# Kernel tuning notes

Measured on AMD Instinct MI355X. Metric: run time of the kernel, lower is better.

The kernel has to match this reference:

```python
import jax, jax.numpy as jnp
import numpy as np

N_NODES = 50000
N_EDGES = 800000
IN_DIM = 1200   # latent_size * num_heads
OUT_DIM = 300
NEG_SLOPE = 0.2  # PyG GATConv default


def setup_inputs() -> dict:
    key = jax.random.key(0)
    k1, k2, k3, k4, k5 = jax.random.split(key, 5)
    z = jax.random.normal(k1, (N_NODES, IN_DIM), dtype=jnp.float32)
    edge_index = jax.random.randint(k2, (2, N_EDGES), 0, N_NODES, dtype=jnp.int64)
    # GATConv params (heads=1): lin weight [out, in], attention vectors [out], bias [out]
    W = jax.random.normal(k3, (OUT_DIM, IN_DIM), dtype=jnp.float32) * (1.0 / np.sqrt(IN_DIM))
    att_src = jax.random.normal(k4, (OUT_DIM,), dtype=jnp.float32) * 0.1
    att_dst = jax.random.normal(k5, (OUT_DIM,), dtype=jnp.float32) * 0.1
    bias = jnp.zeros((OUT_DIM,), dtype=jnp.float32)
    return {"z": z, "edge_index": edge_index, "W": W,
            "att_src": att_src, "att_dst": att_dst, "bias": bias}


def reference(z, edge_index, W, att_src, att_dst, bias):
    N = z.shape[0]
    # Linear projection (no bias on lin in GATConv; bias added after aggregation)
    x = z @ W.T                                   # [N, OUT_DIM]
    # add self-loops (GATConv default add_self_loops=True)
    loop = jnp.arange(N, dtype=edge_index.dtype)
    src = jnp.concatenate([edge_index[0], loop])  # message source j
    dst = jnp.concatenate([edge_index[1], loop])  # message target i
    # per-node attention logits
    a_src = x @ att_src                           # [N]
    a_dst = x @ att_dst                           # [N]
    # per-edge score, softmax over incoming edges of each target node
    e = jax.nn.leaky_relu(a_src[src] + a_dst[dst], negative_slope=NEG_SLOPE)  # [E+N]
    e_max = jax.ops.segment_max(e, dst, num_segments=N)   # every node has a self-loop
    ex = jnp.exp(e - e_max[dst])
    denom = jax.ops.segment_sum(ex, dst, num_segments=N)
    alpha = ex / denom[dst]                       # [E+N]
    # weighted aggregation (scatter-add over targets)
    out = jax.ops.segment_sum(alpha[:, None] * x[src], dst, num_segments=N)
    return out + bias
```

## Files before the change

### kernel.cpp

```cpp
#include <hip/hip_runtime.h>

#define N_NODES 50000
#define N_EDGES 800000
#define IN_DIM  1200
#define KP      1216
#define OUT_DIM 300
#define BNP     320
#define XBS     304
#define BM      64
#define NKT     38
#define GRID_M  ((N_NODES + BM - 1) / BM)

typedef __attribute__((ext_vector_type(8))) short short8;
typedef __attribute__((ext_vector_type(4))) float f32x4;

__device__ __forceinline__ short f2bf(float f) {
  unsigned u = __builtin_bit_cast(unsigned, f);
  u += 0x7fffu + ((u >> 16) & 1u);
  return (short)(u >> 16);
}
__device__ __forceinline__ float bf2f(unsigned short h) {
  return __builtin_bit_cast(float, (unsigned)h << 16);
}
__device__ __forceinline__ float lrelu(float v) { return v > 0.f ? v : 0.2f * v; }

__device__ __forceinline__ float wredMaxF(float v) {
  #pragma unroll
  for (int o = 32; o > 0; o >>= 1) v = fmaxf(v, __shfl_xor(v, o));
  return v;
}
__device__ __forceinline__ float wredSumF(float v) {
  #pragma unroll
  for (int o = 32; o > 0; o >>= 1) v += __shfl_xor(v, o);
  return v;
}

__device__ __forceinline__ void gl_lds16(const unsigned short* g, unsigned short* l) {
  __builtin_amdgcn_global_load_lds(
      (const __attribute__((address_space(1))) unsigned int*)g,
      (__attribute__((address_space(3))) unsigned int*)l, 16, 0, 0);
}

__global__ __launch_bounds__(256) void wconv(const float* __restrict__ W,
                                             unsigned short* __restrict__ Wb) {
  int f = blockIdx.x * 256 + threadIdx.x;
  if (f >= BNP * KP / 8) return;
  int n = (f * 8) / KP, c = (f * 8) % KP;
  short8 v = {0,0,0,0,0,0,0,0};
  if (n < OUT_DIM && c < IN_DIM) {
    const float4* p = reinterpret_cast<const float4*>(W + (size_t)n * IN_DIM + c);
    float4 f0 = p[0], f1 = p[1];
    v[0]=f2bf(f0.x); v[1]=f2bf(f0.y); v[2]=f2bf(f0.z); v[3]=f2bf(f0.w);
    v[4]=f2bf(f1.x); v[5]=f2bf(f1.y); v[6]=f2bf(f1.z); v[7]=f2bf(f1.w);
  }
  *reinterpret_cast<short8*>(&Wb[(size_t)n * KP + c]) = v;
}

__global__ __launch_bounds__(256) void gemm_x(const float* __restrict__ z,
                                              const unsigned short* __restrict__ Wb,
                                              const float* __restrict__ att_s,
                                              const float* __restrict__ att_d,
                                              unsigned short* __restrict__ xb,
                                              float* __restrict__ a_s,
                                              float* __restrict__ a_d) {
  __shared__ __align__(16) unsigned short As[2][BM * 32];
  __shared__ __align__(16) unsigned short Bs[2][BNP * 32];

  const int tid  = threadIdx.x;
  const int lane = tid & 63;
  const int wid  = tid >> 6;
  const int lr   = lane & 15;
  const int lg   = lane >> 4;
  const int lrs  = (lr >> 1) & 3;
  const int m0   = blockIdx.x * BM;

  f32x4 zero4 = {0.f, 0.f, 0.f, 0.f};
  const float4 fz4 = make_float4(0.f, 0.f, 0.f, 0.f);
  f32x4 acc[4][5];
  #pragma unroll
  for (int mf = 0; mf < 4; ++mf)
    #pragma unroll
    for (int nj = 0; nj < 5; ++nj) acc[mf][nj] = zero4;

  const int ra  = tid >> 2;
  const int kaL = tid & 3;
  const int kaP = kaL ^ ((ra >> 1) & 3);
  const int am  = m0 + ra;
  float4 ga0, ga1;

  const int brow = wid * 16 + (lane >> 2);
  const int bgc  = (lane & 3) ^ ((lane >> 3) & 3);

  #define LOADA(KT)                                                           \
    {                                                                         \
      int k = (KT) * 32 + kaL * 8;                                            \
      if (am < N_NODES && k + 8 <= IN_DIM) {                                  \
        const float4* p = reinterpret_cast<const float4*>(z + (size_t)am * IN_DIM + k); \
        ga0 = p[0]; ga1 = p[1];                                               \
      } else { ga0 = fz4; ga1 = fz4; }                                        \
    }

  #define WRITEA(BUF)                                                         \
    {                                                                         \
      short8 v;                                                               \
      v[0]=f2bf(ga0.x); v[1]=f2bf(ga0.y); v[2]=f2bf(ga0.z); v[3]=f2bf(ga0.w); \
      v[4]=f2bf(ga1.x); v[5]=f2bf(ga1.y); v[6]=f2bf(ga1.z); v[7]=f2bf(ga1.w); \
      *reinterpret_cast<short8*>(&As[BUF][ra * 32 + kaP * 8]) = v;            \
    }

  #define STAGEB(BUF, KT)                                                     \
    _Pragma("unroll")                                                         \
    for (int j = 0; j < 5; ++j) {                                             \
      const unsigned short* gsrc =                                            \
          Wb + (size_t)(j * 64 + brow) * KP + (KT) * 32 + bgc * 8;            \
      unsigned short* ldst = &Bs[BUF][(j * 64 + wid * 16) * 32];              \
      gl_lds16(gsrc, ldst);                                                   \
    }

  STAGEB(0, 0);
  LOADA(0);
  WRITEA(0);
  __syncthreads();

  #pragma unroll 1
  for (int kt = 0; kt < NKT; ++kt) {
    const int cur = kt & 1;
    if (kt < NKT - 1) {
      STAGEB(cur ^ 1, kt + 1);
      LOADA(kt + 1);
    }

    short8 a[4];
    #pragma unroll
    for (int mf = 0; mf < 4; ++mf)
      a[mf] = *reinterpret_cast<const short8*>(
          &As[cur][(mf * 16 + lr) * 32 + (lg ^ lrs) * 8]);
    #pragma unroll
    for (int nj = 0; nj < 5; ++nj) {
      short8 b = *reinterpret_cast<const short8*>(
          &Bs[cur][(wid * 80 + nj * 16 + lr) * 32 + (lg ^ lrs) * 8]);
      #pragma unroll
      for (int mf = 0; mf < 4; ++mf)
        acc[mf][nj] = __builtin_amdgcn_mfma_f32_16x16x32_bf16(a[mf], b, acc[mf][nj], 0, 0, 0);
    }

    if (kt < NKT - 1) { WRITEA(cur ^ 1); }
    __syncthreads();
  }
  #undef LOADA
  #undef WRITEA
  #undef STAGEB

  float* red = reinterpret_cast<float*>(&As[0][0]);

  float ps[4][4], pd[4][4];
  #pragma unroll
  for (int mf = 0; mf < 4; ++mf)
    #pragma unroll
    for (int jj = 0; jj < 4; ++jj) { ps[mf][jj] = 0.f; pd[mf][jj] = 0.f; }

  #pragma unroll
  for (int nj = 0; nj < 5; ++nj) {
    int c = wid * 80 + nj * 16 + lr;
    bool cv = c < OUT_DIM;
    float vs = cv ? att_s[c] : 0.f;
    float vd = cv ? att_d[c] : 0.f;
    #pragma unroll
    for (int mf = 0; mf < 4; ++mf) {
      #pragma unroll
      for (int jj = 0; jj < 4; ++jj) {
        float val = acc[mf][nj][jj];
        int r = m0 + mf * 16 + 4 * lg + jj;
        if (cv && r < N_NODES) xb[(size_t)r * XBS + c] = (unsigned short)f2bf(val);
        ps[mf][jj] += val * vs;
        pd[mf][jj] += val * vd;
      }
    }
  }
  #pragma unroll
  for (int mf = 0; mf < 4; ++mf)
    #pragma unroll
    for (int jj = 0; jj < 4; ++jj) {
      #pragma unroll
      for (int o = 8; o > 0; o >>= 1) {
        ps[mf][jj] += __shfl_xor(ps[mf][jj], o);
        pd[mf][jj] += __shfl_xor(pd[mf][jj], o);
      }
      if (lr == 0) {
        int rr = mf * 16 + 4 * lg + jj;
        red[wid * 64 + rr]       = ps[mf][jj];
        red[256 + wid * 64 + rr] = pd[mf][jj];
      }
    }
  __syncthreads();
  if (tid < 64) {
    int r = m0 + tid;
    if (r < N_NODES)
      a_s[r] = red[tid] + red[64 + tid] + red[128 + tid] + red[192 + tid];
  } else if (tid < 128) {
    int t = tid - 64, r = m0 + t;
    if (r < N_NODES)
      a_d[r] = red[256 + t] + red[256 + 64 + t] + red[256 + 128 + t] + red[256 + 192 + t];
  }
}

__global__ void hist(const int* __restrict__ ei, int* __restrict__ deg) {
  int e = blockIdx.x * blockDim.x + threadIdx.x;
  if (e < N_EDGES) {
    unsigned dst = (unsigned)ei[N_EDGES + e];
    if (dst < N_NODES) atomicAdd(&deg[dst], 1);
  }
}

#define SCAN_B 1024
#define NBLK   49

__global__ __launch_bounds__(SCAN_B) void scan1(const int* __restrict__ deg,
                                                int* __restrict__ bsum) {
  int i = blockIdx.x * SCAN_B + threadIdx.x;
  int v = (i < N_NODES) ? deg[i] : 0;
  #pragma unroll
  for (int o = 32; o > 0; o >>= 1) v += __shfl_xor(v, o);
  __shared__ int wt[16];
  if ((threadIdx.x & 63) == 0) wt[threadIdx.x >> 6] = v;
  __syncthreads();
  if (threadIdx.x == 0) {
    int t = 0;
    #pragma unroll
    for (int w = 0; w < 16; ++w) t += wt[w];
    bsum[blockIdx.x] = t;
  }
}

__global__ void scan2(const int* __restrict__ bsum, int* __restrict__ bex,
                      int* __restrict__ offs) {
  int l = threadIdx.x;
  int v = (l < NBLK) ? bsum[l] : 0;
  int incl = v;
  #pragma unroll
  for (int off = 1; off < 64; off <<= 1) {
    int u = __shfl_up(incl, off);
    if (l >= off) incl += u;
  }
  if (l < NBLK) bex[l] = incl - v;
  if (l == NBLK - 1) offs[N_NODES] = incl;
}

__global__ __launch_bounds__(SCAN_B) void scan3(const int* __restrict__ deg,
                                                const int* __restrict__ bex,
                                                int* __restrict__ offs,
                                                int* __restrict__ cursor) {
  int tid = threadIdx.x;
  int i = blockIdx.x * SCAN_B + tid;
  int lane = tid & 63, wid = tid >> 6;
  int v = (i < N_NODES) ? deg[i] : 0;
  int incl = v;
  #pragma unroll
  for (int off = 1; off < 64; off <<= 1) {
    int u = __shfl_up(incl, off);
    if (lane >= off) incl += u;
  }
  __shared__ int wt[16];
  if (lane == 63) wt[wid] = incl;
  __syncthreads();
  if (tid < 16) {
    int t = wt[tid];
    int sc = t;
    #pragma unroll
    for (int off = 1; off < 16; off <<= 1) {
      int u = __shfl_up(sc, off);
      if (tid >= off) sc += u;
    }
    wt[tid] = sc - t;
  }
  __syncthreads();
  int excl = incl - v + wt[wid] + bex[blockIdx.x];
  if (i < N_NODES) { offs[i] = excl; cursor[i] = excl; }
}

__global__ void fill(const int* __restrict__ ei, int* __restrict__ cursor,
                     int* __restrict__ srcs) {
  int e = blockIdx.x * blockDim.x + threadIdx.x;
  if (e < N_EDGES) {
    unsigned dst = (unsigned)ei[N_EDGES + e];
    unsigned src = (unsigned)ei[e];
    if (dst < N_NODES && src < N_NODES) {
      int pos = atomicAdd(&cursor[dst], 1);
      srcs[pos] = (int)src;
    }
  }
}

__global__ __launch_bounds__(256) void minv_k(const float* __restrict__ a_s,
                                              const float* __restrict__ a_d,
                                              const int* __restrict__ offs,
                                              const int* __restrict__ srcs,
                                              float2* __restrict__ minv) {
  int node = blockIdx.x * 4 + (threadIdx.x >> 6);
  if (node >= N_NODES) return;
  int lane = threadIdx.x & 63;
  int beg = offs[node], end = offs[node + 1];
  float adi = a_d[node];
  float eself = lrelu(a_s[node] + adi);

  float m = eself;
  for (int k = beg + lane; k < end; k += 64)
    m = fmaxf(m, lrelu(a_s[srcs[k]] + adi));
  m = wredMaxF(m);

  float s = 0.f;
  for (int k = beg + lane; k < end; k += 64)
    s += expf(lrelu(a_s[srcs[k]] + adi) - m);
  s = wredSumF(s) + expf(eself - m);
  if (lane == 0) minv[node] = make_float2(m, 1.0f / s);
}

#define CCH 15
__global__ __launch_bounds__(256) void aggregate(const unsigned short* __restrict__ xb,
                                                 const float* __restrict__ a_s,
                                                 const float* __restrict__ a_d,
                                                 const float2* __restrict__ minv,
                                                 const int* __restrict__ offs,
                                                 const int* __restrict__ srcs,
                                                 const float* __restrict__ bias,
                                                 float* __restrict__ out) {
  unsigned wi = blockIdx.x * 256u + threadIdx.x;
  if (wi >= (unsigned)N_NODES * CCH) return;
  unsigned node = wi / CCH;
  unsigned cc = wi - node * CCH;

  int beg = offs[node], end = offs[node + 1];
  float2 mi = minv[node];
  const float m = mi.x, inv = mi.y;
  const float adi = a_d[node];
  const float wself = expf(lrelu(a_s[node] + adi) - m) * inv;

  const unsigned short* xcol = xb + 20u * cc;

  float acc[20];
  {
    const unsigned short* xr = xcol + (size_t)node * XBS;
    #pragma unroll
    for (int q = 0; q < 5; ++q) {
      ushort4 xv = *reinterpret_cast<const ushort4*>(xr + 4 * q);
      acc[4*q+0] = wself * bf2f(xv.x);
      acc[4*q+1] = wself * bf2f(xv.y);
      acc[4*q+2] = wself * bf2f(xv.z);
      acc[4*q+3] = wself * bf2f(xv.w);
    }
  }

  for (int k = beg; k < end; ++k) {
    int sj = srcs[k];
    float w = expf(lrelu(a_s[sj] + adi) - m) * inv;
    const unsigned short* xr = xcol + (size_t)sj * XBS;
    #pragma unroll
    for (int q = 0; q < 5; ++q) {
      ushort4 xv = *reinterpret_cast<const ushort4*>(xr + 4 * q);
      acc[4*q+0] += w * bf2f(xv.x);
      acc[4*q+1] += w * bf2f(xv.y);
      acc[4*q+2] += w * bf2f(xv.z);
      acc[4*q+3] += w * bf2f(xv.w);
    }
  }
  float* op = out + (size_t)node * OUT_DIM + 20u * cc;
  const float* bp = bias + 20u * cc;
  #pragma unroll
  for (int q = 0; q < 5; ++q) {
    float4 b = *reinterpret_cast<const float4*>(bp + 4 * q);
    float4 o = {acc[4*q] + b.x, acc[4*q+1] + b.y, acc[4*q+2] + b.z, acc[4*q+3] + b.w};
    *reinterpret_cast<float4*>(op + 4 * q) = o;
  }
}

extern "C" void kernel_launch(void* const* d_in, const int* in_sizes, int n_in,
                              void* d_out, int out_size, void* d_ws, size_t ws_size,
                              hipStream_t stream) {
  const float* z     = (const float*)d_in[0];
  const int*   ei    = (const int*)d_in[1];
  const float* W     = (const float*)d_in[2];
  const float* att_s = (const float*)d_in[3];
  const float* att_d = (const float*)d_in[4];
  const float* bias  = (const float*)d_in[5];
  float* out = (float*)d_out;

  char* ws = (char*)d_ws;
  size_t off = 0;
  unsigned short* xb = (unsigned short*)(ws + off); off += (size_t)N_NODES * XBS * 2;
  unsigned short* Wb = (unsigned short*)(ws + off); off += (size_t)BNP * KP * 2;
  float*  a_s  = (float*)(ws + off);  off += 50048 * 4;
  float*  a_d  = (float*)(ws + off);  off += 50048 * 4;
  int*    deg  = (int*)(ws + off);    off += 50048 * 4;
  int*    offs = (int*)(ws + off);    off += 50056 * 4;
  int*    cur  = (int*)(ws + off);    off += 50048 * 4;
  int*    bsum = (int*)(ws + off);    off += 64 * 4;
  int*    bex  = (int*)(ws + off);    off += 64 * 4;
  int*    srcs = (int*)(ws + off);    off += (size_t)N_EDGES * 4;
  float2* minv = (float2*)(ws + off); off += (size_t)50048 * 8;

  (void)hipMemsetAsync(deg, 0, N_NODES * 4, stream);

  wconv<<<(BNP * KP / 8 + 255) / 256, 256, 0, stream>>>(W, Wb);
  gemm_x<<<GRID_M, 256, 0, stream>>>(z, Wb, att_s, att_d, xb, a_s, a_d);
  hist<<<(N_EDGES + 255) / 256, 256, 0, stream>>>(ei, deg);
  scan1<<<NBLK, SCAN_B, 0, stream>>>(deg, bsum);
  scan2<<<1, 64, 0, stream>>>(bsum, bex, offs);
  scan3<<<NBLK, SCAN_B, 0, stream>>>(deg, bex, offs, cur);
  fill<<<(N_EDGES + 255) / 256, 256, 0, stream>>>(ei, cur, srcs);
  minv_k<<<(N_NODES + 3) / 4, 256, 0, stream>>>(a_s, a_d, offs, srcs, minv);
  aggregate<<<((unsigned)N_NODES * CCH + 255) / 256, 256, 0, stream>>>(
      xb, a_s, a_d, minv, offs, srcs, bias, out);
}
```

Before: 329.3 us.

## Deepen GEMM pipeline with two-tile A register prefetch and manual waitcnt barriers

Restructures the projection GEMM main loop into a manually unrolled two-stage ping-pong where global A loads run two k-tiles ahead in alternating register sets. __syncthreads is replaced by explicit s_waitcnt vmcnt(2) plus s_barrier, so the latest A prefetch can stay in flight across the barrier. Out-of-range loads become clamped unconditional loads with zero-masking applied at the LDS write. The aim is to hide global-load latency behind MFMA work. In exchange it uses more registers and depends on hand-counted vmcnt values being correct.

```diff
diff --git a/kernel.cpp b/kernel.cpp
--- a/kernel.cpp
+++ b/kernel.cpp
@@ -86,25 +86,28 @@
   const int kaL = tid & 3;
   const int kaP = kaL ^ ((ra >> 1) & 3);
   const int am  = m0 + ra;
-  float4 ga0, ga1;
-
-  const int brow = wid * 16 + (lane >> 2);
-  const int bgc  = (lane & 3) ^ ((lane >> 3) & 3);
-
-  #define LOADA(KT)                                                           \
+  const int amc = am < N_NODES ? am : N_NODES - 1;
+  const bool mok = am < N_NODES;
+
+  float4 gA0, gA1, gB0, gB1;
+
+  const int bgc = (lane & 3) ^ ((lane >> 3) & 3);
+
+  #define LOADA(G0, G1, KT)                                                   \
     {                                                                         \
       int k = (KT) * 32 + kaL * 8;                                            \
-      if (am < N_NODES && k + 8 <= IN_DIM) {                                  \
-        const float4* p = reinterpret_cast<const float4*>(z + (size_t)am * IN_DIM + k); \
-        ga0 = p[0]; ga1 = p[1];                                               \
-      } else { ga0 = fz4; ga1 = fz4; }                                        \
-    }
-
-  #define WRITEA(BUF)                                                         \
+      int kc = k > (IN_DIM - 8) ? (IN_DIM - 8) : k;                           \
+      const float4* p = reinterpret_cast<const float4*>(z + (size_t)amc * IN_DIM + kc); \
+      G0 = p[0]; G1 = p[1];                                                   \
+    }
+
+  #define WRITEA(BUF, G0, G1, KT)                                             \
     {                                                                         \
+      bool ok = mok && ((KT) * 32 + kaL * 8 + 8 <= IN_DIM);                   \
+      float4 f0 = ok ? G0 : fz4, f1 = ok ? G1 : fz4;                          \
       short8 v;                                                               \
-      v[0]=f2bf(ga0.x); v[1]=f2bf(ga0.y); v[2]=f2bf(ga0.z); v[3]=f2bf(ga0.w); \
-      v[4]=f2bf(ga1.x); v[5]=f2bf(ga1.y); v[6]=f2bf(ga1.z); v[7]=f2bf(ga1.w); \
+      v[0]=f2bf(f0.x); v[1]=f2bf(f0.y); v[2]=f2bf(f0.z); v[3]=f2bf(f0.w);     \
+      v[4]=f2bf(f1.x); v[5]=f2bf(f1.y); v[6]=f2bf(f1.z); v[7]=f2bf(f1.w);     \
       *reinterpret_cast<short8*>(&As[BUF][ra * 32 + kaP * 8]) = v;            \
     }
 
@@ -112,44 +115,75 @@
     _Pragma("unroll")                                                         \
     for (int j = 0; j < 5; ++j) {                                             \
       const unsigned short* gsrc =                                            \
-          Wb + (size_t)(j * 64 + brow) * KP + (KT) * 32 + bgc * 8;            \
-      unsigned short* ldst = &Bs[BUF][(j * 64 + wid * 16) * 32];              \
-      gl_lds16(gsrc, ldst);                                                   \
-    }
-
+          Wb + (size_t)(j * 64 + wid * 16 + (lane >> 2)) * KP + (KT) * 32 + bgc * 8; \
+      gl_lds16(gsrc, &Bs[BUF][(j * 64 + wid * 16) * 32]);                     \
+    }
+
+  #define COMPUTE(CUR)                                                        \
+    {                                                                         \
+      short8 a0_ = *reinterpret_cast<const short8*>(&As[CUR][(lr) * 32 + (lg ^ lrs) * 8]);        \
+      short8 a1_ = *reinterpret_cast<const short8*>(&As[CUR][(16 + lr) * 32 + (lg ^ lrs) * 8]);   \
+      short8 a2_ = *reinterpret_cast<const short8*>(&As[CUR][(32 + lr) * 32 + (lg ^ lrs) * 8]);   \
+      short8 a3_ = *reinterpret_cast<const short8*>(&As[CUR][(48 + lr) * 32 + (lg ^ lrs) * 8]);   \
+      _Pragma("unroll")                                                       \
+      for (int nj = 0; nj < 5; ++nj) {                                        \
+        short8 b = *reinterpret_cast<const short8*>(                          \
+            &Bs[CUR][(wid * 80 + nj * 16 + lr) * 32 + (lg ^ lrs) * 8]);       \
+        acc[0][nj] = __builtin_amdgcn_mfma_f32_16x16x32_bf16(a0_, b, acc[0][nj], 0, 0, 0); \
+        acc[1][nj] = __builtin_amdgcn_mfma_f32_16x16x32_bf16(a1_, b, acc[1][nj], 0, 0, 0); \
+        acc[2][nj] = __builtin_amdgcn_mfma_f32_16x16x32_bf16(a2_, b, acc[2][nj], 0, 0, 0); \
+        acc[3][nj] = __builtin_amdgcn_mfma_f32_16x16x32_bf16(a3_, b, acc[3][nj], 0, 0, 0); \
+      }                                                                       \
+    }
+
+  #define FENCE asm volatile("" ::: "memory")
+  #define CBAR  asm volatile("s_waitcnt vmcnt(2) lgkmcnt(0)" ::: "memory");   \
+                __builtin_amdgcn_s_barrier();                                 \
+                asm volatile("" ::: "memory")
+
+  LOADA(gA0, gA1, 0);
+  FENCE;
   STAGEB(0, 0);
-  LOADA(0);
-  WRITEA(0);
-  __syncthreads();
+  FENCE;
+  LOADA(gB0, gB1, 1);
+  FENCE;
+  WRITEA(0, gA0, gA1, 0);
+  CBAR;
 
   #pragma unroll 1
-  for (int kt = 0; kt < NKT; ++kt) {
-    const int cur = kt & 1;
-    if (kt < NKT - 1) {
-      STAGEB(cur ^ 1, kt + 1);
-      LOADA(kt + 1);
-    }
-
-    short8 a[4];
-    #pragma unroll
-    for (int mf = 0; mf < 4; ++mf)
-      a[mf] = *reinterpret_cast<const short8*>(
-          &As[cur][(mf * 16 + lr) * 32 + (lg ^ lrs) * 8]);
-    #pragma unroll
-    for (int nj = 0; nj < 5; ++nj) {
-      short8 b = *reinterpret_cast<const short8*>(
-          &Bs[cur][(wid * 80 + nj * 16 + lr) * 32 + (lg ^ lrs) * 8]);
-      #pragma unroll
-      for (int mf = 0; mf < 4; ++mf)
-        acc[mf][nj] = __builtin_amdgcn_mfma_f32_16x16x32_bf16(a[mf], b, acc[mf][nj], 0, 0, 0);
-    }
-
-    if (kt < NKT - 1) { WRITEA(cur ^ 1); }
-    __syncthreads();
-  }
+  for (int kt = 0; kt < 36; kt += 2) {
+    STAGEB(1, kt + 1);
+    FENCE;
+    LOADA(gA0, gA1, kt + 2);
+    FENCE;
+    COMPUTE(0);
+    WRITEA(1, gB0, gB1, kt + 1);
+    CBAR;
+
+    STAGEB(0, kt + 2);
+    FENCE;
+    LOADA(gB0, gB1, kt + 3);
+    FENCE;
+    COMPUTE(1);
+    WRITEA(0, gA0, gA1, kt + 2);
+    CBAR;
+  }
+
+  STAGEB(1, 37);
+  FENCE;
+  COMPUTE(0);
+  WRITEA(1, gB0, gB1, 37);
+  __syncthreads();
+
+  COMPUTE(1);
+  __syncthreads();
+
   #undef LOADA
   #undef WRITEA
   #undef STAGEB
+  #undef COMPUTE
+  #undef FENCE
+  #undef CBAR
 
   float* red = reinterpret_cast<float*>(&As[0][0]);
 
```

Result: slower. 338.6 us (+2.8%).

## Double GEMM row tile to 128 with 8 waves sharing each staged W tile

Applied to the files above, without the earlier changes.

The projection GEMM now uses 128-row blocks with 512 threads arranged as 2 row-waves by 4 column-waves. Each staged B (weight) tile in LDS is reused across twice as many rows, which halves the number of blocks and the total W traffic from global memory. B staging is redistributed across the 8 waves, and the attention-logit reduction is re-indexed for 128 rows. This costs a larger A buffer in LDS and fewer blocks (391), which may leave the GPU's compute units unevenly loaded.

```diff
diff --git a/kernel.cpp b/kernel.cpp
--- a/kernel.cpp
+++ b/kernel.cpp
@@ -7,7 +7,7 @@
 #define OUT_DIM 300
 #define BNP     320
 #define XBS     304
-#define BM      64
+#define BM      128
 #define NKT     38
 #define GRID_M  ((N_NODES + BM - 1) / BM)
 
@@ -56,7 +56,7 @@
   *reinterpret_cast<short8*>(&Wb[(size_t)n * KP + c]) = v;
 }
 
-__global__ __launch_bounds__(256) void gemm_x(const float* __restrict__ z,
+__global__ __launch_bounds__(512) void gemm_x(const float* __restrict__ z,
                                               const unsigned short* __restrict__ Wb,
                                               const float* __restrict__ att_s,
                                               const float* __restrict__ att_d,
@@ -69,6 +69,8 @@
   const int tid  = threadIdx.x;
   const int lane = tid & 63;
   const int wid  = tid >> 6;
+  const int mw   = wid >> 2;
+  const int nw   = wid & 3;
   const int lr   = lane & 15;
   const int lg   = lane >> 4;
   const int lrs  = (lr >> 1) & 3;
@@ -88,8 +90,7 @@
   const int am  = m0 + ra;
   float4 ga0, ga1;
 
-  const int brow = wid * 16 + (lane >> 2);
-  const int bgc  = (lane & 3) ^ ((lane >> 3) & 3);
+  const int bgc = (lane & 3) ^ ((lane >> 3) & 3);
 
   #define LOADA(KT)                                                           \
     {                                                                         \
@@ -110,11 +111,13 @@
 
   #define STAGEB(BUF, KT)                                                     \
     _Pragma("unroll")                                                         \
-    for (int j = 0; j < 5; ++j) {                                             \
-      const unsigned short* gsrc =                                            \
-          Wb + (size_t)(j * 64 + brow) * KP + (KT) * 32 + bgc * 8;            \
-      unsigned short* ldst = &Bs[BUF][(j * 64 + wid * 16) * 32];              \
-      gl_lds16(gsrc, ldst);                                                   \
+    for (int t5 = 0; t5 < 3; ++t5) {                                          \
+      int j = wid + 8 * t5;                                                   \
+      if (j < 20) {                                                           \
+        const unsigned short* gsrc =                                          \
+            Wb + (size_t)(j * 16 + (lane >> 2)) * KP + (KT) * 32 + bgc * 8;   \
+        gl_lds16(gsrc, &Bs[BUF][j * 16 * 32]);                                \
+      }                                                                       \
     }
 
   STAGEB(0, 0);
@@ -130,18 +133,18 @@
       LOADA(kt + 1);
     }
 
-    short8 a[4];
-    #pragma unroll
-    for (int mf = 0; mf < 4; ++mf)
-      a[mf] = *reinterpret_cast<const short8*>(
-          &As[cur][(mf * 16 + lr) * 32 + (lg ^ lrs) * 8]);
+    short8 a0 = *reinterpret_cast<const short8*>(&As[cur][(mw * 64 +      lr) * 32 + (lg ^ lrs) * 8]);
+    short8 a1 = *reinterpret_cast<const short8*>(&As[cur][(mw * 64 + 16 + lr) * 32 + (lg ^ lrs) * 8]);
+    short8 a2 = *reinterpret_cast<const short8*>(&As[cur][(mw * 64 + 32 + lr) * 32 + (lg ^ lrs) * 8]);
+    short8 a3 = *reinterpret_cast<const short8*>(&As[cur][(mw * 64 + 48 + lr) * 32 + (lg ^ lrs) * 8]);
     #pragma unroll
     for (int nj = 0; nj < 5; ++nj) {
       short8 b = *reinterpret_cast<const short8*>(
-          &Bs[cur][(wid * 80 + nj * 16 + lr) * 32 + (lg ^ lrs) * 8]);
-      #pragma unroll
-      for (int mf = 0; mf < 4; ++mf)
-        acc[mf][nj] = __builtin_amdgcn_mfma_f32_16x16x32_bf16(a[mf], b, acc[mf][nj], 0, 0, 0);
+          &Bs[cur][(nw * 80 + nj * 16 + lr) * 32 + (lg ^ lrs) * 8]);
+      acc[0][nj] = __builtin_amdgcn_mfma_f32_16x16x32_bf16(a0, b, acc[0][nj], 0, 0, 0);
+      acc[1][nj] = __builtin_amdgcn_mfma_f32_16x16x32_bf16(a1, b, acc[1][nj], 0, 0, 0);
+      acc[2][nj] = __builtin_amdgcn_mfma_f32_16x16x32_bf16(a2, b, acc[2][nj], 0, 0, 0);
+      acc[3][nj] = __builtin_amdgcn_mfma_f32_16x16x32_bf16(a3, b, acc[3][nj], 0, 0, 0);
     }
 
     if (kt < NKT - 1) { WRITEA(cur ^ 1); }
@@ -161,7 +164,7 @@
 
   #pragma unroll
   for (int nj = 0; nj < 5; ++nj) {
-    int c = wid * 80 + nj * 16 + lr;
+    int c = nw * 80 + nj * 16 + lr;
     bool cv = c < OUT_DIM;
     float vs = cv ? att_s[c] : 0.f;
     float vd = cv ? att_d[c] : 0.f;
@@ -170,7 +173,7 @@
       #pragma unroll
       for (int jj = 0; jj < 4; ++jj) {
         float val = acc[mf][nj][jj];
-        int r = m0 + mf * 16 + 4 * lg + jj;
+        int r = m0 + mw * 64 + mf * 16 + 4 * lg + jj;
         if (cv && r < N_NODES) xb[(size_t)r * XBS + c] = (unsigned short)f2bf(val);
         ps[mf][jj] += val * vs;
         pd[mf][jj] += val * vd;
@@ -187,20 +190,20 @@
         pd[mf][jj] += __shfl_xor(pd[mf][jj], o);
       }
       if (lr == 0) {
-        int rr = mf * 16 + 4 * lg + jj;
-        red[wid * 64 + rr]       = ps[mf][jj];
-        red[256 + wid * 64 + rr] = pd[mf][jj];
+        int rr = mw * 64 + mf * 16 + 4 * lg + jj;
+        red[nw * 128 + rr]       = ps[mf][jj];
+        red[512 + nw * 128 + rr] = pd[mf][jj];
       }
     }
   __syncthreads();
-  if (tid < 64) {
+  if (tid < 128) {
     int r = m0 + tid;
     if (r < N_NODES)
-      a_s[r] = red[tid] + red[64 + tid] + red[128 + tid] + red[192 + tid];
-  } else if (tid < 128) {
-    int t = tid - 64, r = m0 + t;
+      a_s[r] = red[tid] + red[128 + tid] + red[256 + tid] + red[384 + tid];
+  } else if (tid < 256) {
+    int t = tid - 128, r = m0 + t;
     if (r < N_NODES)
-      a_d[r] = red[256 + t] + red[256 + 64 + t] + red[256 + 128 + t] + red[256 + 192 + t];
+      a_d[r] = red[512 + t] + red[512 + 128 + t] + red[512 + 256 + t] + red[512 + 384 + t];
   }
 }
 
@@ -401,7 +404,7 @@
   (void)hipMemsetAsync(deg, 0, N_NODES * 4, stream);
 
   wconv<<<(BNP * KP / 8 + 255) / 256, 256, 0, stream>>>(W, Wb);
-  gemm_x<<<GRID_M, 256, 0, stream>>>(z, Wb, att_s, att_d, xb, a_s, a_d);
+  gemm_x<<<GRID_M, 512, 0, stream>>>(z, Wb, att_s, att_d, xb, a_s, a_d);
   hist<<<(N_EDGES + 255) / 256, 256, 0, stream>>>(ei, deg);
   scan1<<<NBLK, SCAN_B, 0, stream>>>(deg, bsum);
   scan2<<<1, 64, 0, stream>>>(bsum, bex, offs);
```

Result: no change. 332.0 us (+0.8%).

## Load W fragments directly from global and shrink GEMM M-tile to 48

Applied to the files above, without the earlier changes.

The projection GEMM no longer stages the bf16 weight tile in LDS with global_load_lds. Each wave now reads its B fragments straight from global memory into registers every k-step. The M tile drops from 64 to 48 rows, which means more blocks and lower LDS use, and the z-tile loader is rewritten for 4-wide chunks. The aim is higher occupancy and less LDS traffic, at the cost of redundant global or L2 reads of W across blocks and waves and possible exposed load latency.

```diff
diff --git a/kernel.cpp b/kernel.cpp
--- a/kernel.cpp
+++ b/kernel.cpp
@@ -7,11 +7,12 @@
 #define OUT_DIM 300
 #define BNP     320
 #define XBS     304
-#define BM      64
+#define BM      48
 #define NKT     38
 #define GRID_M  ((N_NODES + BM - 1) / BM)
 
 typedef __attribute__((ext_vector_type(8))) short short8;
+typedef __attribute__((ext_vector_type(4))) short short4v;
 typedef __attribute__((ext_vector_type(4))) float f32x4;
 
 __device__ __forceinline__ short f2bf(float f) {
@@ -33,12 +34,6 @@
   #pragma unroll
   for (int o = 32; o > 0; o >>= 1) v += __shfl_xor(v, o);
   return v;
-}
-
-__device__ __forceinline__ void gl_lds16(const unsigned short* g, unsigned short* l) {
-  __builtin_amdgcn_global_load_lds(
-      (const __attribute__((address_space(1))) unsigned int*)g,
-      (__attribute__((address_space(3))) unsigned int*)l, 16, 0, 0);
 }
 
 __global__ __launch_bounds__(256) void wconv(const float* __restrict__ W,
@@ -64,7 +59,6 @@
                                               float* __restrict__ a_s,
                                               float* __restrict__ a_d) {
   __shared__ __align__(16) unsigned short As[2][BM * 32];
-  __shared__ __align__(16) unsigned short Bs[2][BNP * 32];
 
   const int tid  = threadIdx.x;
   const int lane = tid & 63;
@@ -76,48 +70,47 @@
 
   f32x4 zero4 = {0.f, 0.f, 0.f, 0.f};
   const float4 fz4 = make_float4(0.f, 0.f, 0.f, 0.f);
-  f32x4 acc[4][5];
-  #pragma unroll
-  for (int mf = 0; mf < 4; ++mf)
+  f32x4 acc[3][5];
+  #pragma unroll
+  for (int mf = 0; mf < 3; ++mf)
     #pragma unroll
     for (int nj = 0; nj < 5; ++nj) acc[mf][nj] = zero4;
 
-  const int ra  = tid >> 2;
-  const int kaL = tid & 3;
-  const int kaP = kaL ^ ((ra >> 1) & 3);
-  const int am  = m0 + ra;
+  const int r0_ = tid >> 3,         f0_ = tid & 7;
+  const int r1_ = (tid + 256) >> 3, f1_ = (tid + 256) & 7;
+  const bool has2 = tid < 128;
   float4 ga0, ga1;
 
-  const int brow = wid * 16 + (lane >> 2);
-  const int bgc  = (lane & 3) ^ ((lane >> 3) & 3);
+  const unsigned short* bp = Wb + (size_t)(80 * wid + lr) * KP + lg * 8;
 
   #define LOADA(KT)                                                           \
     {                                                                         \
-      int k = (KT) * 32 + kaL * 8;                                            \
-      if (am < N_NODES && k + 8 <= IN_DIM) {                                  \
-        const float4* p = reinterpret_cast<const float4*>(z + (size_t)am * IN_DIM + k); \
-        ga0 = p[0]; ga1 = p[1];                                               \
-      } else { ga0 = fz4; ga1 = fz4; }                                        \
+      int k0 = (KT) * 32 + f0_ * 4;                                           \
+      int m  = m0 + r0_;                                                      \
+      ga0 = (m < N_NODES && k0 + 4 <= IN_DIM)                                 \
+        ? *reinterpret_cast<const float4*>(z + (size_t)m * IN_DIM + k0) : fz4;\
+      if (has2) {                                                             \
+        int k1 = (KT) * 32 + f1_ * 4;                                         \
+        int m1 = m0 + r1_;                                                    \
+        ga1 = (m1 < N_NODES && k1 + 4 <= IN_DIM)                              \
+          ? *reinterpret_cast<const float4*>(z + (size_t)m1 * IN_DIM + k1) : fz4; \
+      }                                                                       \
     }
 
   #define WRITEA(BUF)                                                         \
     {                                                                         \
-      short8 v;                                                               \
+      short4v v;                                                              \
       v[0]=f2bf(ga0.x); v[1]=f2bf(ga0.y); v[2]=f2bf(ga0.z); v[3]=f2bf(ga0.w); \
-      v[4]=f2bf(ga1.x); v[5]=f2bf(ga1.y); v[6]=f2bf(ga1.z); v[7]=f2bf(ga1.w); \
-      *reinterpret_cast<short8*>(&As[BUF][ra * 32 + kaP * 8]) = v;            \
-    }
-
-  #define STAGEB(BUF, KT)                                                     \
-    _Pragma("unroll")                                                         \
-    for (int j = 0; j < 5; ++j) {                                             \
-      const unsigned short* gsrc =                                            \
-          Wb + (size_t)(j * 64 + brow) * KP + (KT) * 32 + bgc * 8;            \
-      unsigned short* ldst = &Bs[BUF][(j * 64 + wid * 16) * 32];              \
-      gl_lds16(gsrc, ldst);                                                   \
-    }
-
-  STAGEB(0, 0);
+      int c2 = (f0_ >> 1) ^ ((r0_ >> 1) & 3);                                 \
+      *reinterpret_cast<short4v*>(&As[BUF][r0_ * 32 + c2 * 8 + (f0_ & 1) * 4]) = v; \
+      if (has2) {                                                             \
+        short4v w2;                                                           \
+        w2[0]=f2bf(ga1.x); w2[1]=f2bf(ga1.y); w2[2]=f2bf(ga1.z); w2[3]=f2bf(ga1.w); \
+        int c3 = (f1_ >> 1) ^ ((r1_ >> 1) & 3);                               \
+        *reinterpret_cast<short4v*>(&As[BUF][r1_ * 32 + c3 * 8 + (f1_ & 1) * 4]) = w2; \
+      }                                                                       \
+    }
+
   LOADA(0);
   WRITEA(0);
   __syncthreads();
@@ -125,37 +118,49 @@
   #pragma unroll 1
   for (int kt = 0; kt < NKT; ++kt) {
     const int cur = kt & 1;
+    if (kt < NKT - 1) { LOADA(kt + 1); }
+
+    const unsigned short* bk = bp + kt * 32;
+    short8 b0 = *reinterpret_cast<const short8*>(bk);
+    short8 b1 = *reinterpret_cast<const short8*>(bk + (size_t)16 * KP);
+    short8 b2 = *reinterpret_cast<const short8*>(bk + (size_t)32 * KP);
+    short8 b3 = *reinterpret_cast<const short8*>(bk + (size_t)48 * KP);
+    short8 b4 = *reinterpret_cast<const short8*>(bk + (size_t)64 * KP);
+
+    short8 a0 = *reinterpret_cast<const short8*>(&As[cur][(lr) * 32 + (lg ^ lrs) * 8]);
+    short8 a1 = *reinterpret_cast<const short8*>(&As[cur][(16 + lr) * 32 + (lg ^ lrs) * 8]);
+    short8 a2 = *reinterpret_cast<const short8*>(&As[cur][(32 + lr) * 32 + (lg ^ lrs) * 8]);
+
+    acc[0][0] = __builtin_amdgcn_mfma_f32_16x16x32_bf16(a0, b0, acc[0][0], 0, 0, 0);
+    acc[1][0] = __builtin_amdgcn_mfma_f32_16x16x32_bf16(a1, b0, acc[1][0], 0, 0, 0);
+    acc[2][0] = __builtin_amdgcn_mfma_f32_16x16x32_bf16(a2, b0, acc[2][0], 0, 0, 0);
+    acc[0][1] = __builtin_amdgcn_mfma_f32_16x16x32_bf16(a0, b1, acc[0][1], 0, 0, 0);
+    acc[1][1] = __builtin_amdgcn_mfma_f32_16x16x32_bf16(a1, b1, acc[1][1], 0, 0, 0);
+    acc[2][1] = __builtin_amdgcn_mfma_f32_16x16x32_bf16(a2, b1, acc[2][1], 0, 0, 0);
+    acc[0][2] = __builtin_amdgcn_mfma_f32_16x16x32_bf16(a0, b2, acc[0][2], 0, 0, 0);
+    acc[1][2] = __builtin_amdgcn_mfma_f32_16x16x32_bf16(a1, b2, acc[1][2], 0, 0, 0);
+    acc[2][2] = __builtin_amdgcn_mfma_f32_16x16x32_bf16(a2, b2, acc[2][2], 0, 0, 0);
+    acc[0][3] = __builtin_amdgcn_mfma_f32_16x16x32_bf16(a0, b3, acc[0][3], 0, 0, 0);
+    acc[1][3] = __builtin_amdgcn_mfma_f32_16x16x32_bf16(a1, b3, acc[1][3], 0, 0, 0);
+    acc[2][3] = __builtin_amdgcn_mfma_f32_16x16x32_bf16(a2, b3, acc[2][3], 0, 0, 0);
+    acc[0][4] = __builtin_amdgcn_mfma_f32_16x16x32_bf16(a0, b4, acc[0][4], 0, 0, 0);
+    acc[1][4] = __builtin_amdgcn_mfma_f32_16x16x32_bf16(a1, b4, acc[1][4], 0, 0, 0);
+    acc[2][4] = __builtin_amdgcn_mfma_f32_16x16x32_bf16(a2, b4, acc[2][4], 0, 0, 0);
+
     if (kt < NKT - 1) {
-      STAGEB(cur ^ 1, kt + 1);
-      LOADA(kt + 1);
-    }
-
-    short8 a[4];
-    #pragma unroll
-    for (int mf = 0; mf < 4; ++mf)
-      a[mf] = *reinterpret_cast<const short8*>(
-          &As[cur][(mf * 16 + lr) * 32 + (lg ^ lrs) * 8]);
-    #pragma unroll
-    for (int nj = 0; nj < 5; ++nj) {
-      short8 b = *reinterpret_cast<const short8*>(
-          &Bs[cur][(wid * 80 + nj * 16 + lr) * 32 + (lg ^ lrs) * 8]);
-      #pragma unroll
-      for (int mf = 0; mf < 4; ++mf)
-        acc[mf][nj] = __builtin_amdgcn_mfma_f32_16x16x32_bf16(a[mf], b, acc[mf][nj], 0, 0, 0);
-    }
-
-    if (kt < NKT - 1) { WRITEA(cur ^ 1); }
-    __syncthreads();
+      WRITEA(cur ^ 1);
+      __syncthreads();
+    }
   }
   #undef LOADA
   #undef WRITEA
-  #undef STAGEB
-
+
+  __syncthreads();
   float* red = reinterpret_cast<float*>(&As[0][0]);
 
-  float ps[4][4], pd[4][4];
-  #pragma unroll
-  for (int mf = 0; mf < 4; ++mf)
+  float ps[3][4], pd[3][4];
+  #pragma unroll
+  for (int mf = 0; mf < 3; ++mf)
     #pragma unroll
     for (int jj = 0; jj < 4; ++jj) { ps[mf][jj] = 0.f; pd[mf][jj] = 0.f; }
 
@@ -166,7 +171,7 @@
     float vs = cv ? att_s[c] : 0.f;
     float vd = cv ? att_d[c] : 0.f;
     #pragma unroll
-    for (int mf = 0; mf < 4; ++mf) {
+    for (int mf = 0; mf < 3; ++mf) {
       #pragma unroll
       for (int jj = 0; jj < 4; ++jj) {
         float val = acc[mf][nj][jj];
@@ -178,7 +183,7 @@
     }
   }
   #pragma unroll
-  for (int mf = 0; mf < 4; ++mf)
+  for (int mf = 0; mf < 3; ++mf)
     #pragma unroll
     for (int jj = 0; jj < 4; ++jj) {
       #pragma unroll
@@ -188,19 +193,19 @@
       }
       if (lr == 0) {
         int rr = mf * 16 + 4 * lg + jj;
-        red[wid * 64 + rr]       = ps[mf][jj];
-        red[256 + wid * 64 + rr] = pd[mf][jj];
+        red[wid * 48 + rr]       = ps[mf][jj];
+        red[192 + wid * 48 + rr] = pd[mf][jj];
       }
     }
   __syncthreads();
-  if (tid < 64) {
+  if (tid < 48) {
     int r = m0 + tid;
     if (r < N_NODES)
-      a_s[r] = red[tid] + red[64 + tid] + red[128 + tid] + red[192 + tid];
-  } else if (tid < 128) {
-    int t = tid - 64, r = m0 + t;
+      a_s[r] = red[tid] + red[48 + tid] + red[96 + tid] + red[144 + tid];
+  } else if (tid < 96) {
+    int t = tid - 48, r = m0 + t;
     if (r < N_NODES)
-      a_d[r] = red[256 + t] + red[256 + 64 + t] + red[256 + 128 + t] + red[256 + 192 + t];
+      a_d[r] = red[192 + t] + red[192 + 48 + t] + red[192 + 96 + t] + red[192 + 144 + t];
   }
 }
 
```

Result: slower. 454.1 us (+37.9%).
